# Kernel optimization log

Measured on AMD Instinct MI355X. Metric: run time of the kernel, lower is better.

## Reference

```python
import jax, jax.numpy as jnp
import numpy as np
from math import factorial as _f

MAX_L = 2
NUM_CHANNELS = 64
B, N, C = 4, 1024, 64


def _cg_coeff(l1, m1, l2, m2, L, M):
    # Standard real Clebsch-Gordan coefficient <l1 m1 l2 m2 | L M> (Condon-Shortley)
    if m1 + m2 != M or not (abs(l1 - l2) <= L <= l1 + l2):
        return 0.0
    pre = ((2 * L + 1) * _f(L + l1 - l2) * _f(L - l1 + l2) * _f(l1 + l2 - L) / _f(l1 + l2 + L + 1)) ** 0.5
    pre *= (_f(L + M) * _f(L - M) * _f(l1 - m1) * _f(l1 + m1) * _f(l2 - m2) * _f(l2 + m2)) ** 0.5
    s = 0.0
    for k in range(0, l1 + l2 - L + 1):
        dens = [k, l1 + l2 - L - k, l1 - m1 - k, l2 + m2 - k, L - l2 + m1 + k, L - l1 - m2 + k]
        if any(d < 0 for d in dens):
            continue
        term = (-1.0) ** k
        for d in dens:
            term /= _f(d)
        s += term
    return pre * s


def _cg_tensor(l1, l2, L):
    # dense CG block [2l1+1, 2l2+1, 2L+1]
    T = np.zeros((2 * l1 + 1, 2 * l2 + 1, 2 * L + 1), np.float32)
    for i, m1 in enumerate(range(-l1, l1 + 1)):
        for j, m2 in enumerate(range(-l2, l2 + 1)):
            for k, M in enumerate(range(-L, L + 1)):
                T[i, j, k] = _cg_coeff(l1, m1, l2, m2, L, M)
    return jnp.asarray(T)


# precompute small CG blocks once (tiny, static)
_CG = {(l1, l2, L): _cg_tensor(l1, l2, L)
       for l1 in range(MAX_L + 1) for l2 in range(MAX_L + 1)
       for L in range(MAX_L + 1) if abs(l1 - l2) <= L <= l1 + l2}


def setup_inputs() -> dict:
    key = jax.random.key(0)
    ks = jax.random.split(key, 7)
    inp = {}
    for l, k in zip(range(MAX_L + 1), ks[:3]):
        inp[f"v{l}"] = jax.random.normal(k, (B, N, 2 * l + 1, C), jnp.float32)
    for l, k in zip(range(MAX_L + 1), ks[3:6]):
        inp[f"s{l}"] = jax.random.normal(k, (B, N, N, 2 * l + 1, 1), jnp.float32)
    inp["conn"] = jax.random.randint(ks[6], (B, N, N), 0, 2, jnp.int32)
    return inp


def reference(v0, v1, v2, s0, s1, s2, conn):
    v = [v0, v1, v2]
    sph = [s0, s1, s2]
    # sphx.parts[l] = einsum('bijmc->bimc', sph.parts[l]) : sum over neighbor index j
    sx = [jnp.einsum('bijmc->bimc', s) for s in sph]
    adj = conn.astype(v0.dtype)  # [B,N,N] gather mask (Rmask1)

    # CGproduct(vertices, sphx): for each output degree L, concat all (l1,l2) fragments
    cg_parts = []
    for L in range(MAX_L + 1):
        frags = []
        for l1 in range(MAX_L + 1):
            for l2 in range(MAX_L + 1):
                if abs(l1 - l2) <= L <= l1 + l2:
                    # [B,N,2L+1,C*1]
                    o = jnp.einsum('bnic,bnjd,ijk->bnkcd', v[l1], sx[l2], _CG[(l1, l2, L)])
                    frags.append(o.reshape(o.shape[0], o.shape[1], 2 * L + 1, -1))
        cg_parts.append(jnp.concatenate(frags, axis=-1))

    # message passing: sum-gather over connected neighbors
    mp = [jnp.einsum('bnm,bmkc->bnkc', adj, p) for p in cg_parts]

    # per-l normalization: divide by (2l+1)*||part||_F / num_channels
    normed = []
    for L, p in enumerate(mp):
        nf = (2 * L + 1) * jnp.linalg.norm(p)
        normed.append(p / (nf / NUM_CHANNELS))

    # flatten (m, channel) per degree and concat for a single output array
    return jnp.concatenate([p.reshape(p.shape[0], p.shape[1], -1) for p in normed], axis=-1)
```

## Files before the change

### kernel.cpp

```cpp
#include <hip/hip_runtime.h>
#include <math.h>

typedef __attribute__((ext_vector_type(8))) short short8;
typedef __attribute__((ext_vector_type(4))) float f32x4;

#define B_   4
#define N_   1024
#define FTOT 3264
#define FPAD 3328

#define WS_SS   0
#define WS_CG   256
#define WS_SX   4096
#define WS_ABF  151552
#define WS_PT   8540160

__device__ __forceinline__ unsigned short f2bf(float x) {
  union { float f; unsigned u; } v; v.f = x;
  unsigned r = v.u + 0x7FFFu + ((v.u >> 16) & 1u);
  return (unsigned short)(r >> 16);
}

__device__ __forceinline__ void gload16(const void* gp, void* lp) {
  __builtin_amdgcn_global_load_lds((const __attribute__((address_space(1))) unsigned int*)gp,
                                   (__attribute__((address_space(3))) unsigned int*)lp, 16, 0, 0);
}

__device__ __forceinline__ float wave_sum(float v) {
#pragma unroll
  for (int off = 32; off > 0; off >>= 1) v += __shfl_down(v, off, 64);
  return v;
}

__device__ double dfact(int n) { double r = 1.0; for (int i = 2; i <= n; ++i) r *= (double)i; return r; }

__device__ float cg_coeff(int l1, int m1, int l2, int m2, int L, int M) {
  if (m1 + m2 != M) return 0.f;
  int dl = l1 - l2; if (dl < 0) dl = -dl;
  if (L < dl || L > l1 + l2) return 0.f;
  double pre = sqrt((double)(2*L+1) * dfact(L+l1-l2) * dfact(L-l1+l2) * dfact(l1+l2-L) / dfact(l1+l2+L+1));
  pre *= sqrt(dfact(L+M)*dfact(L-M)*dfact(l1-m1)*dfact(l1+m1)*dfact(l2-m2)*dfact(l2+m2));
  double s = 0.0;
  for (int k = 0; k <= l1 + l2 - L; ++k) {
    int d1 = l1+l2-L-k, d2 = l1-m1-k, d3 = l2+m2-k, d4 = L-l2+m1+k, d5 = L-l1-m2+k;
    if (d1 < 0 || d2 < 0 || d3 < 0 || d4 < 0 || d5 < 0) continue;
    double t = (k & 1) ? -1.0 : 1.0;
    t /= dfact(k)*dfact(d1)*dfact(d2)*dfact(d3)*dfact(d4)*dfact(d5);
    s += t;
  }
  return (float)(pre * s);
}

__device__ const int t_l1[15]  = {0,1,2, 0,1,1,1,2,2, 0,1,1,2,2,2};
__device__ const int t_l2[15]  = {0,1,2, 1,0,1,2,1,2, 2,1,2,0,1,2};
__device__ const int t_L [15]  = {0,0,0, 1,1,1,1,1,1, 2,2,2,2,2,2};
__device__ const int t_off[16] = {0,1,10, 35,44,53,80,125,170, 245,270,315,390,415,490, 615};

__device__ const int d_l1[3][6]  = {{0,1,2,0,0,0},{0,1,1,1,2,2},{0,1,1,2,2,2}};
__device__ const int d_l2[3][6]  = {{0,1,2,0,0,0},{1,0,1,2,1,2},{2,1,2,0,1,2}};
__device__ const int d_off[3][6] = {{0,1,10,0,0,0},{35,44,53,80,125,170},{245,270,315,390,415,490}};
__device__ const int d_rb[3] = {0, 1, 4};

__global__ __launch_bounds__(256) void k_pre(const float* __restrict__ s0p, const float* __restrict__ s1p,
                                             const float* __restrict__ s2p, float* __restrict__ sx,
                                             const int* __restrict__ conn, unsigned short* __restrict__ Abf,
                                             float* __restrict__ ss, float* __restrict__ cg) {
  __shared__ float red[9][256];
  const int tid = threadIdx.x;

  if (blockIdx.x < 4096) {
    const int bn = blockIdx.x;
    const f32x4* p0 = (const f32x4*)(s0p + (size_t)bn * 1024);
    const f32x4* p1 = (const f32x4*)(s1p + (size_t)bn * 3072);
    const f32x4* p2 = (const f32x4*)(s2p + (size_t)bn * 5120);

    f32x4 va = p0[tid];
    f32x4 vb[3];
#pragma unroll
    for (int it = 0; it < 3; ++it) vb[it] = p1[tid + 256 * it];
    f32x4 vc[5];
#pragma unroll
    for (int it = 0; it < 5; ++it) vc[it] = p2[tid + 256 * it];

    float a = va[0] + va[1] + va[2] + va[3];

    float b[3] = {0.f, 0.f, 0.f};
#pragma unroll
    for (int it = 0; it < 3; ++it)
#pragma unroll
      for (int e = 0; e < 4; ++e)
        b[(it + e) % 3] += vb[it][e];

    float c[5] = {0.f, 0.f, 0.f, 0.f, 0.f};
#pragma unroll
    for (int it = 0; it < 5; ++it)
#pragma unroll
      for (int e = 0; e < 4; ++e)
        c[(4 * it + e) % 5] += vc[it][e];

    red[0][tid] = a;
    const int r3 = tid % 3;
#pragma unroll
    for (int u = 0; u < 3; ++u) red[1 + (r3 + u) % 3][tid] = b[u];
    const int q5 = (4 * tid) % 5;
#pragma unroll
    for (int u = 0; u < 5; ++u) red[4 + (q5 + u) % 5][tid] = c[u];
    __syncthreads();

    const int lane = tid & 63, w = tid >> 6;
    for (int r = w; r < 9; r += 4) {
      float v = red[r][lane] + red[r][lane + 64] + red[r][lane + 128] + red[r][lane + 192];
      v = wave_sum(v);
      if (lane == 0) sx[(size_t)bn * 9 + r] = v;
    }
    return;
  }

  const int idx  = (blockIdx.x - 4096) * 256 + tid;
  const int lane = idx & 63;
  const int w    = (idx >> 6) & 2047;
  const int b    = idx >> 17;
  const int nt16 = w >> 5;
  const int ks   = w & 31;
  const int l16  = lane & 15, quad = lane >> 4;
  const int n    = nt16 * 16 + l16;
  const int m8   = ks * 32 + quad * 8;
  const int4* src = (const int4*)(conn + ((size_t)(b * 1024 + n) * 1024 + m8));
  int4 c0 = src[0], c1 = src[1];
  short8 o;
  o[0] = f2bf((float)c0.x); o[1] = f2bf((float)c0.y);
  o[2] = f2bf((float)c0.z); o[3] = f2bf((float)c0.w);
  o[4] = f2bf((float)c1.x); o[5] = f2bf((float)c1.y);
  o[6] = f2bf((float)c1.z); o[7] = f2bf((float)c1.w);
  const int nt = n >> 7, nr = n & 127;
  *(short8*)&Abf[(size_t)(b * 8 + nt) * 131072 + ks * 4096 +
                 ((nr >> 4) * 4 + quad) * 128 + (nr & 15) * 8] = o;

  if (blockIdx.x == 4096) {
    if (tid < 4) ss[tid] = 0.f;
    for (int t0 = tid; t0 < 615; t0 += 256) {
      int t = 0;
      while (t < 14 && t0 >= t_off[t+1]) ++t;
      int local = t0 - t_off[t];
      int l1 = t_l1[t], l2 = t_l2[t], L = t_L[t];
      int nk = 2*L+1, n2 = 2*l2+1;
      int k = local % nk; int rest = local / nk;
      int j = rest % n2;  int i = rest / n2;
      cg[t0] = cg_coeff(l1, i - l1, l2, j - l2, L, k - L);
    }
  }
}

#define VSTRIDE 148

template <int L>
__device__ __forceinline__ void cg_emit(const float* __restrict__ vme, const float sxr[9],
                                        const float* __restrict__ cgt,
                                        unsigned short* __restrict__ pout, int cbase) {
  const int nfrag = (L == 0) ? 3 : 6;
  const int nk = 2 * L + 1;
  const int Lbase = (L == 0) ? 0 : (L == 1 ? 192 : 1344);
  const int Cfrag = nfrag * 64;
#pragma unroll
  for (int frag = 0; frag < nfrag; ++frag) {
    const int l1 = d_l1[L][frag], l2 = d_l2[L][frag];
    const int n1 = 2 * l1 + 1, n2 = 2 * l2 + 1;
    const int rb1 = d_rb[l1], rb2 = d_rb[l2];
    const int cgo = d_off[L][frag];
#pragma unroll
    for (int k = 0; k < nk; ++k) {
      float w[5];
#pragma unroll
      for (int i = 0; i < n1; ++i) {
        float a = 0.f;
#pragma unroll
        for (int j = 0; j < n2; ++j)
          a += sxr[rb2 + j] * cgt[cgo + (i * n2 + j) * nk + k];
        w[i] = a;
      }
      f32x4 val = {0.f, 0.f, 0.f, 0.f};
#pragma unroll
      for (int i = 0; i < n1; ++i) {
        f32x4 vv = *(const f32x4*)(vme + (rb1 + i) * 16);
        val += vv * w[i];
      }
      const int fb = Lbase + k * Cfrag + frag * 64 + cbase;
      const int ftile = fb >> 7, fr = fb & 127;
      unsigned short* pp = pout + (size_t)ftile * 131072 + (fr >> 4) * 512 + (fr & 15) * 8;
#pragma unroll
      for (int cc = 0; cc < 4; ++cc)
        pp[cc * 8] = f2bf(val[cc]);
    }
  }
}

__global__ __launch_bounds__(256) void k_cgp(const float* __restrict__ v0, const float* __restrict__ v1,
                                             const float* __restrict__ v2, const float* __restrict__ sx,
                                             const float* __restrict__ cgt, unsigned short* __restrict__ Pt) {
  __shared__ float vsh[64 * VSTRIDE];
  const int half = blockIdx.x & 1;
  const int cq   = blockIdx.x >> 1;
  const int mt   = blockIdx.y;
  const int b    = blockIdx.z;
  const int m0 = mt * 64;
  const int c0 = cq * 16;
  const int tid = threadIdx.x;
  const size_t nb = (size_t)b * N_ + m0;

  {
    const int mloc = tid >> 2;
    const int cc0  = (tid & 3) * 4;
    const size_t vrow = nb + mloc;
    *(f32x4*)&vsh[mloc*VSTRIDE + 0*16 + cc0] = *(const f32x4*)&v0[vrow * 64 + c0 + cc0];
#pragma unroll
    for (int r = 1; r < 4; ++r)
      *(f32x4*)&vsh[mloc*VSTRIDE + r*16 + cc0] = *(const f32x4*)&v1[(vrow * 3 + (r-1)) * 64 + c0 + cc0];
#pragma unroll
    for (int r = 4; r < 9; ++r)
      *(f32x4*)&vsh[mloc*VSTRIDE + r*16 + cc0] = *(const f32x4*)&v2[(vrow * 5 + (r-4)) * 64 + c0 + cc0];
  }
  const int lane = tid & 63, wv = tid >> 6;
  float sxr[9];
#pragma unroll
  for (int r = 0; r < 9; ++r) sxr[r] = sx[(nb + lane) * 9 + r];
  __syncthreads();

  const int ks = mt * 2 + (lane >> 5);
  const int kq = ((lane & 31) >> 3) * 128 + (lane & 7);
  unsigned short* pout = Pt + (size_t)b * 26 * 131072 + ks * 4096 + kq;
  const int cbase = c0 + wv * 4;
  const float* vme = &vsh[lane * VSTRIDE + wv * 4];

  if (half == 0) {
    cg_emit<0>(vme, sxr, cgt, pout, cbase);
    cg_emit<1>(vme, sxr, cgt, pout, cbase);
  } else {
    cg_emit<2>(vme, sxr, cgt, pout, cbase);
    const int fr = 64 + cbase;
    unsigned short* pp = pout + (size_t)25 * 131072 + (fr >> 4) * 512 + (fr & 15) * 8;
#pragma unroll
    for (int cc = 0; cc < 4; ++cc)
      pp[cc * 8] = 0;
  }
}

#define WAIT_VM8 0x0F78
#define WAIT_VM0 0x0F70

__global__ __launch_bounds__(512, 2) void k_gemm(const unsigned short* __restrict__ PtT,
                                                 const unsigned short* __restrict__ AbT,
                                                 float* __restrict__ out, float* __restrict__ ssv) {
  __shared__ unsigned short As[2][2][8192];
  __shared__ unsigned short Bs[2][2][8192];
  const int i  = blockIdx.x;
  const int x  = i & 7, j = i >> 3;
  const int b   = x >> 1;
  const int ntp = 2 * (x & 1) + (j & 1);
  const int ftp = j >> 1;
  const int f0 = ftp * 256, n0 = ntp * 256;
  const int tid  = threadIdx.x;
  const int w    = tid >> 6, lane = tid & 63;
  const int wr   = w >> 2, wc = w & 3;
  const int l16  = lane & 15, quad = lane >> 4;

  const unsigned short* gA0 = PtT + (size_t)(b * 26 + 2 * ftp    ) * 131072;
  const unsigned short* gA1 = PtT + (size_t)(b * 26 + 2 * ftp + 1) * 131072;
  const unsigned short* gB0 = AbT + (size_t)(b * 8  + 2 * ntp    ) * 131072;
  const unsigned short* gB1 = AbT + (size_t)(b * 8  + 2 * ntp + 1) * 131072;
  const int so = w * 512 + lane * 8;

#define ISSUE(T, BUF) do { \
    const size_t o = (size_t)(T) * 8192 + so; \
    gload16(gA0 + o,        &As[BUF][0][w * 512]); \
    gload16(gA0 + o + 4096, &As[BUF][0][4096 + w * 512]); \
    gload16(gA1 + o,        &As[BUF][1][w * 512]); \
    gload16(gA1 + o + 4096, &As[BUF][1][4096 + w * 512]); \
    gload16(gB0 + o,        &Bs[BUF][0][w * 512]); \
    gload16(gB0 + o + 4096, &Bs[BUF][0][4096 + w * 512]); \
    gload16(gB1 + o,        &Bs[BUF][1][w * 512]); \
    gload16(gB1 + o + 4096, &Bs[BUF][1][4096 + w * 512]); \
  } while (0)

  f32x4 acc[8][4] = {};
  const int bh  = wc >> 1;
  const int bl4 = (wc & 1) * 4;

#define COMPUTE(BUF) do { \
    _Pragma("unroll") \
    for (int kc = 0; kc < 2; ++kc) { \
      short8 bf[4]; \
      _Pragma("unroll") \
      for (int ni = 0; ni < 4; ++ni) \
        bf[ni] = *(const short8*)&Bs[BUF][bh][kc*4096 + ((bl4 + ni)*4 + quad)*128 + l16*8]; \
      _Pragma("unroll") \
      for (int mh = 0; mh < 2; ++mh) { \
        short8 af[4]; \
        _Pragma("unroll") \
        for (int m = 0; m < 4; ++m) \
          af[m] = *(const short8*)&As[BUF][wr][kc*4096 + ((mh*4 + m)*4 + quad)*128 + l16*8]; \
        _Pragma("unroll") \
        for (int m = 0; m < 4; ++m) \
          _Pragma("unroll") \
          for (int ni = 0; ni < 4; ++ni) \
            acc[mh*4 + m][ni] = __builtin_amdgcn_mfma_f32_16x16x32_bf16(af[m], bf[ni], acc[mh*4 + m][ni], 0, 0, 0); \
      } \
    } \
  } while (0)

  ISSUE(0, 0);
  ISSUE(1, 1);
  for (int t = 0; t < 15; ++t) {
    const int buf = t & 1;
    __builtin_amdgcn_s_waitcnt(WAIT_VM8);
    __builtin_amdgcn_s_barrier();
    COMPUTE(buf);
    __builtin_amdgcn_s_barrier();
    if (t < 14) ISSUE(t + 2, buf);
  }
  __builtin_amdgcn_s_waitcnt(WAIT_VM0);
  __builtin_amdgcn_s_barrier();
  COMPUTE(1);

  float ssl0 = 0.f, ssl1 = 0.f, ssl2 = 0.f;
#pragma unroll
  for (int mi = 0; mi < 8; ++mi) {
    const int fbase = f0 + wr*128 + mi*16 + quad*4;
    if (fbase >= FTOT) continue;
    float sq = 0.f;
#pragma unroll
    for (int ni = 0; ni < 4; ++ni) {
      const int n = n0 + wc*64 + ni*16 + l16;
      f32x4 v = acc[mi][ni];
      sq += v[0]*v[0] + v[1]*v[1] + v[2]*v[2] + v[3]*v[3];
      *(f32x4*)&out[((size_t)b * N_ + n) * FTOT + fbase] = v;
    }
    if (fbase < 192) ssl0 += sq; else if (fbase < 1344) ssl1 += sq; else ssl2 += sq;
  }
  ssl0 = wave_sum(ssl0); ssl1 = wave_sum(ssl1); ssl2 = wave_sum(ssl2);

  __syncthreads();
  float* red = (float*)&As[0][0][0];
  if (lane == 0) { red[w*3 + 0] = ssl0; red[w*3 + 1] = ssl1; red[w*3 + 2] = ssl2; }
  __syncthreads();
  if (tid < 3) {
    float s = 0.f;
#pragma unroll
    for (int ww = 0; ww < 8; ++ww) s += red[ww*3 + tid];
    if (s != 0.f) atomicAdd(&ssv[tid], s);
  }
#undef ISSUE
#undef COMPUTE
}

__global__ __launch_bounds__(256) void k_scale(float* __restrict__ out, const float* __restrict__ ssv) {
  const int idx = blockIdx.x * 256 + threadIdx.x;
  const int total = B_ * N_ * (FTOT / 4);
  if (idx >= total) return;
  const int f = (idx % (FTOT / 4)) * 4;
  const int L = f < 192 ? 0 : (f < 1344 ? 1 : 2);
  const float sc = 64.f / ((float)(2*L+1) * sqrtf(ssv[L]));
  f32x4* p = (f32x4*)out + idx;
  f32x4 v = *p;
  v *= sc;
  *p = v;
}

extern "C" void kernel_launch(void* const* d_in, const int* in_sizes, int n_in,
                              void* d_out, int out_size, void* d_ws, size_t ws_size,
                              hipStream_t stream) {
  const float* v0 = (const float*)d_in[0];
  const float* v1 = (const float*)d_in[1];
  const float* v2 = (const float*)d_in[2];
  const float* s0 = (const float*)d_in[3];
  const float* s1 = (const float*)d_in[4];
  const float* s2 = (const float*)d_in[5];
  const int* conn = (const int*)d_in[6];
  char* ws = (char*)d_ws;
  float* ss            = (float*)(ws + WS_SS);
  float* cg            = (float*)(ws + WS_CG);
  float* sx            = (float*)(ws + WS_SX);
  unsigned short* Abf  = (unsigned short*)(ws + WS_ABF);
  unsigned short* Pt   = (unsigned short*)(ws + WS_PT);
  float* out = (float*)d_out;

  k_pre  <<<dim3(6144),         dim3(256), 0, stream>>>(s0, s1, s2, sx, conn, Abf, ss, cg);
  k_cgp  <<<dim3(8, 16, B_),    dim3(256), 0, stream>>>(v0, v1, v2, sx, cg, Pt);
  k_gemm <<<dim3(208),          dim3(512), 0, stream>>>(Pt, Abf, out, ss);
  k_scale<<<dim3(13056),        dim3(256), 0, stream>>>(out, ss);
}
```

Measured before the change: 277.8 us.

## Fuse normalization scaling into GEMM epilogue via a grid-wide atomic barrier

Drops the separate k_scale kernel. Each GEMM block now adds its partial sum of squares, then waits on a global atomic counter until all 208 blocks have arrived. It then reads the final norms and writes already-scaled outputs from registers. This removes a full read-modify-write pass over the ~53MB output and one kernel launch. The cost is a spin-wait grid barrier, which relies on all blocks being co-resident, and a counter at ssv[3] that must be reset every call.

Result: no change. 273.3 us (-1.6%).

```diff
diff --git a/kernel.cpp b/kernel.cpp
--- a/kernel.cpp
+++ b/kernel.cpp
@@ -246,6 +246,7 @@
 
 #define WAIT_VM8 0x0F78
 #define WAIT_VM0 0x0F70
+#define NBLK 208
 
 __global__ __launch_bounds__(512, 2) void k_gemm(const unsigned short* __restrict__ PtT,
                                                  const unsigned short* __restrict__ AbT,
@@ -329,40 +330,54 @@
     float sq = 0.f;
 #pragma unroll
     for (int ni = 0; ni < 4; ++ni) {
+      f32x4 v = acc[mi][ni];
+      sq += v[0]*v[0] + v[1]*v[1] + v[2]*v[2] + v[3]*v[3];
+    }
+    if (fbase < 192) ssl0 += sq; else if (fbase < 1344) ssl1 += sq; else ssl2 += sq;
+  }
+  ssl0 = wave_sum(ssl0); ssl1 = wave_sum(ssl1); ssl2 = wave_sum(ssl2);
+
+  __syncthreads();
+  float* red = (float*)&As[0][0][0];
+  if (lane == 0) { red[w*3 + 0] = ssl0; red[w*3 + 1] = ssl1; red[w*3 + 2] = ssl2; }
+  __syncthreads();
+  if (tid < 3) {
+    float s = 0.f;
+#pragma unroll
+    for (int ww = 0; ww < 8; ++ww) s += red[ww*3 + tid];
+    if (s != 0.f) atomicAdd(&ssv[tid], s);
+  }
+  __syncthreads();
+
+  int* cnt = (int*)(ssv + 3);
+  if (tid == 0) {
+    __threadfence();
+    atomicAdd(cnt, 1);
+    while (atomicAdd(cnt, 0) < NBLK) __builtin_amdgcn_s_sleep(8);
+  }
+  __syncthreads();
+
+  if (tid < 3) red[tid] = atomicAdd(&ssv[tid], 0.f);
+  __syncthreads();
+  const float sc0 = 64.f / (1.f * sqrtf(red[0]));
+  const float sc1 = 64.f / (3.f * sqrtf(red[1]));
+  const float sc2 = 64.f / (5.f * sqrtf(red[2]));
+
+#pragma unroll
+  for (int mi = 0; mi < 8; ++mi) {
+    const int fbase = f0 + wr*128 + mi*16 + quad*4;
+    if (fbase >= FTOT) continue;
+    const float sc = fbase < 192 ? sc0 : (fbase < 1344 ? sc1 : sc2);
+#pragma unroll
+    for (int ni = 0; ni < 4; ++ni) {
       const int n = n0 + wc*64 + ni*16 + l16;
       f32x4 v = acc[mi][ni];
-      sq += v[0]*v[0] + v[1]*v[1] + v[2]*v[2] + v[3]*v[3];
+      v *= sc;
       *(f32x4*)&out[((size_t)b * N_ + n) * FTOT + fbase] = v;
     }
-    if (fbase < 192) ssl0 += sq; else if (fbase < 1344) ssl1 += sq; else ssl2 += sq;
-  }
-  ssl0 = wave_sum(ssl0); ssl1 = wave_sum(ssl1); ssl2 = wave_sum(ssl2);
-
-  __syncthreads();
-  float* red = (float*)&As[0][0][0];
-  if (lane == 0) { red[w*3 + 0] = ssl0; red[w*3 + 1] = ssl1; red[w*3 + 2] = ssl2; }
-  __syncthreads();
-  if (tid < 3) {
-    float s = 0.f;
-#pragma unroll
-    for (int ww = 0; ww < 8; ++ww) s += red[ww*3 + tid];
-    if (s != 0.f) atomicAdd(&ssv[tid], s);
   }
 #undef ISSUE
 #undef COMPUTE
-}
-
-__global__ __launch_bounds__(256) void k_scale(float* __restrict__ out, const float* __restrict__ ssv) {
-  const int idx = blockIdx.x * 256 + threadIdx.x;
-  const int total = B_ * N_ * (FTOT / 4);
-  if (idx >= total) return;
-  const int f = (idx % (FTOT / 4)) * 4;
-  const int L = f < 192 ? 0 : (f < 1344 ? 1 : 2);
-  const float sc = 64.f / ((float)(2*L+1) * sqrtf(ssv[L]));
-  f32x4* p = (f32x4*)out + idx;
-  f32x4 v = *p;
-  v *= sc;
-  *p = v;
 }
 
 extern "C" void kernel_launch(void* const* d_in, const int* in_sizes, int n_in,
@@ -386,5 +401,4 @@
   k_pre  <<<dim3(6144),         dim3(256), 0, stream>>>(s0, s1, s2, sx, conn, Abf, ss, cg);
   k_cgp  <<<dim3(8, 16, B_),    dim3(256), 0, stream>>>(v0, v1, v2, sx, cg, Pt);
   k_gemm <<<dim3(208),          dim3(512), 0, stream>>>(Pt, Abf, out, ss);
-  k_scale<<<dim3(13056),        dim3(256), 0, stream>>>(out, ss);
-}
+}
```
